# Performance work log

Hardware: AMD Instinct MI355X
Metric: run time of the kernel (lower is better)

The kernel has to match this reference:

```python
import math
import jax, jax.numpy as jnp
import numpy as np

B, T, DIN, D, L, H = 512, 16, 7, 512, 2, 8
FF = 4 * D
HD = D // H
NEG = -1e30


def setup_inputs() -> dict:
    key = jax.random.key(0)
    ks = jax.random.split(key, 18)
    s = 0.02
    n = lambda k, sh: jax.random.normal(k, sh, dtype=jnp.float32) * s
    return {
        "x_scalar_norm": jax.random.normal(ks[0], (B, T, DIN), dtype=jnp.float32),
        "ip_w": n(ks[1], (DIN, D)),   # input_proj (x @ W)
        "ip_b": n(ks[2], (D,)),
        "qkv_w": n(ks[3], (L, D, 3 * D)),  # packed in_proj per layer
        "qkv_b": n(ks[4], (L, 3 * D)),
        "out_w": n(ks[5], (L, D, D)),
        "out_b": n(ks[6], (L, D)),
        "ln1_s": jnp.ones((L, D), jnp.float32),
        "ln1_b": jnp.zeros((L, D), jnp.float32),
        "ff_w1": n(ks[7], (L, D, FF)),
        "ff_b1": n(ks[8], (L, FF)),
        "ff_w2": n(ks[9], (L, FF, D)),
        "ff_b2": n(ks[10], (L, D)),
        "ln2_s": jnp.ones((L, D), jnp.float32),
        "ln2_b": jnp.zeros((L, D), jnp.float32),
        "head_w": n(ks[11], (D, 3)),  # moment_head
        "head_b": n(ks[12], (3,)),
    }


def _pos_encoding(t, d):
    pos = jnp.arange(t, dtype=jnp.float32)[:, None]
    div = jnp.exp(jnp.arange(0, d, 2, dtype=jnp.float32) * (-math.log(10000.0) / d))
    pe = jnp.zeros((t, d), jnp.float32)
    pe = pe.at[:, 0::2].set(jnp.sin(pos * div))
    pe = pe.at[:, 1::2].set(jnp.cos(pos * div))
    return pe


def _ln(x, s, b, eps=1e-5):
    m = jnp.mean(x, axis=-1, keepdims=True)
    v = jnp.mean(jnp.square(x - m), axis=-1, keepdims=True)
    return (x - m) * jax.lax.rsqrt(v + eps) * s + b


def _encoder_layer(h, qkv_w, qkv_b, out_w, out_b, ln1_s, ln1_b,
                   w1, b1, w2, b2, ln2_s, ln2_b, causal):
    b, t, _ = h.shape
    qkv = h @ qkv_w + qkv_b  # [b, t, 3D]
    q, k, v = jnp.split(qkv, 3, axis=-1)
    q = q.reshape(b, t, H, HD).transpose(0, 2, 1, 3)  # bhqd
    k = k.reshape(b, t, H, HD).transpose(0, 2, 1, 3)
    v = v.reshape(b, t, H, HD).transpose(0, 2, 1, 3)
    scores = jnp.einsum('bhqd,bhkd->bhqk', q, k) / math.sqrt(HD)
    scores = jnp.where(causal[None, None], scores, NEG)
    attn = jax.nn.softmax(scores, axis=-1)
    o = jnp.einsum('bhqk,bhkd->bhqd', attn, v)
    o = o.transpose(0, 2, 1, 3).reshape(b, t, D) @ out_w + out_b
    h = _ln(h + o, ln1_s, ln1_b)           # post-norm (norm_first=False)
    ff = jax.nn.relu(h @ w1 + b1) @ w2 + b2
    return _ln(h + ff, ln2_s, ln2_b)


def reference(x_scalar_norm, ip_w, ip_b, qkv_w, qkv_b, out_w, out_b,
              ln1_s, ln1_b, ff_w1, ff_b1, ff_w2, ff_b2, ln2_s, ln2_b,
              head_w, head_b):
    b, t_total, _ = x_scalar_norm.shape
    pe = _pos_encoding(t_total, D)
    x_roll = x_scalar_norm
    preds = []
    for t in range(t_total):
        xp = x_roll[:, :t + 1, :]                 # full backbone recompute per step
        h = xp @ ip_w + ip_b + pe[None, :t + 1]
        causal = jnp.tril(jnp.ones((t + 1, t + 1), dtype=bool))
        for l in range(L):
            h = _encoder_layer(h, qkv_w[l], qkv_b[l], out_w[l], out_b[l],
                               ln1_s[l], ln1_b[l], ff_w1[l], ff_b1[l],
                               ff_w2[l], ff_b2[l], ln2_s[l], ln2_b[l], causal)
        y_t = h[:, -1, :] @ head_w + head_b       # [b, 3]
        preds.append(y_t)
        if t < t_total - 1:
            # eval mode: no teacher forcing; feed back detached prediction
            x_roll = x_roll.at[:, t + 1, DIN - 3:].set(jax.lax.stop_gradient(y_t))
    return jnp.stack(preds, axis=1)  # [b, T, 3]
```

## Files before the change

kernel.cpp:

```cpp
#include <hip/hip_runtime.h>
#include <hip/hip_bf16.h>
#include <math.h>


typedef __attribute__((__ext_vector_type__(8))) short short8;
typedef __attribute__((__ext_vector_type__(4))) float floatx4;

__device__ inline short8 as_short8(uint4 v){ union U{uint4 u; short8 s;} x; x.u=v; return x.s; }

__device__ inline ushort f2bf(float f){
    __hip_bfloat16 h = __float2bfloat16(f);
    ushort u; __builtin_memcpy(&u, &h, 2); return u;
}

__global__ __launch_bounds__(256)
void swz_k(const float* __restrict__ qkv_w, const float* __restrict__ out_w,
           const float* __restrict__ ff1_w, const float* __restrict__ ff2_w,
           ushort* __restrict__ wsw)
{
    int id = blockIdx.z; int l = id & 1; int mi = id >> 1;
    int K, N; const float* src; size_t doff;
    if (mi == 0)      { K = 512;  N = 1536; src = qkv_w + (size_t)l*786432;  doff = (size_t)l*786432; }
    else if (mi == 1) { K = 512;  N = 512;  src = out_w + (size_t)l*262144;  doff = 1572864 + (size_t)l*262144; }
    else if (mi == 2) { K = 512;  N = 2048; src = ff1_w + (size_t)l*1048576; doff = 2097152 + (size_t)l*1048576; }
    else              { K = 2048; N = 512;  src = ff2_w + (size_t)l*1048576; doff = 4194304 + (size_t)l*1048576; }
    int n0 = blockIdx.x * 64, k0 = blockIdx.y * 32;
    if (n0 >= N || k0 >= K) return;
    __shared__ float tt[32][64];
    int tid = threadIdx.x;
    int c = tid & 63, r = tid >> 6;
    #pragma unroll
    for (int i = 0; i < 8; ++i)
        tt[r + i*4][c] = src[(size_t)(k0 + r + i*4)*N + n0 + c];
    __syncthreads();
    int q = tid >> 6, n = tid & 63;
    union { ushort s[8]; uint4 v; } pk;
    #pragma unroll
    for (int i = 0; i < 8; ++i) pk.s[i] = f2bf(tt[q*8 + i][n]);
    ((uint4*)(wsw + doff))[(size_t)((k0 >> 5)*4 + q)*N + n0 + n] = pk.v;
}

__global__ __launch_bounds__(256)
void embed0_k(const float* __restrict__ x, const float* __restrict__ ip_w,
              const float* __restrict__ ip_b, float* __restrict__ h,
              __hip_bfloat16* __restrict__ hbf)
{
    int idx = blockIdx.x*256 + threadIdx.x;
    int b = idx >> 9, d = idx & 511;
    float pe = (d & 1) ? 1.0f : 0.0f;
    float acc = ip_b[d] + pe;
    #pragma unroll
    for (int i = 0; i < 7; ++i)
        acc += x[(b*16 + 0)*7 + i] * ip_w[i*512 + d];
    h[idx] = acc;
    hbf[idx] = __float2bfloat16(acc);
}

template<int MODE>
__global__ __launch_bounds__(256)
void gemm64_k(const __hip_bfloat16* __restrict__ A, const ushort* __restrict__ Wsw,
              const float* __restrict__ bias, int t,
              float* __restrict__ qbuf, __hip_bfloat16* __restrict__ kc,
              __hip_bfloat16* __restrict__ vc,
              __hip_bfloat16* __restrict__ obf, float* __restrict__ ofp,
              const float* __restrict__ resid)
{
    constexpr int K = (MODE == 2) ? 2048 : 512;
    constexpr int N = (MODE == 0) ? 1536 : (MODE == 1 ? 2048 : 512);
    __shared__ uint4 ldsA[256], ldsB[256];
    int tid = threadIdx.x, lane = tid & 63, w = tid >> 6;
    int n0 = blockIdx.x*64, m0 = blockIdx.y*64;
    const uint4* Ag = (const uint4*)A;
    const uint4* Bg = (const uint4*)Wsw;
    int am = tid >> 2, aq = tid & 3;
    int bq = tid >> 6, bn = tid & 63;
    int rh = w & 1, ch = w >> 1;
    int qd = lane >> 4, ln = lane & 15;
    floatx4 a00 = {}, a01 = {}, a10 = {}, a11 = {};
    for (int kb = 0; kb < K/32; ++kb){
        ldsA[aq*64 + am] = Ag[(size_t)(m0 + am)*(K/8) + kb*4 + aq];
        ldsB[bq*64 + bn] = Bg[(size_t)(kb*4 + bq)*N + n0 + bn];
        __syncthreads();
        short8 af0 = as_short8(ldsA[qd*64 + rh*32 +      ln]);
        short8 af1 = as_short8(ldsA[qd*64 + rh*32 + 16 + ln]);
        short8 bf0 = as_short8(ldsB[qd*64 + ch*32 +      ln]);
        short8 bf1 = as_short8(ldsB[qd*64 + ch*32 + 16 + ln]);
        a00 = __builtin_amdgcn_mfma_f32_16x16x32_bf16(af0, bf0, a00, 0, 0, 0);
        a01 = __builtin_amdgcn_mfma_f32_16x16x32_bf16(af0, bf1, a01, 0, 0, 0);
        a10 = __builtin_amdgcn_mfma_f32_16x16x32_bf16(af1, bf0, a10, 0, 0, 0);
        a11 = __builtin_amdgcn_mfma_f32_16x16x32_bf16(af1, bf1, a11, 0, 0, 0);
        __syncthreads();
    }
    floatx4 accs[2][2] = {{a00, a01}, {a10, a11}};
    #pragma unroll
    for (int i = 0; i < 2; ++i){
        #pragma unroll
        for (int j = 0; j < 2; ++j){
            #pragma unroll
            for (int r = 0; r < 4; ++r){
                int m = m0 + rh*32 + i*16 + qd*4 + r;
                int n = n0 + ch*32 + j*16 + ln;
                float v = accs[i][j][r] + bias[n];
                if (MODE == 0){
                    if (n < 512) qbuf[(size_t)m*512 + n] = v;
                    else if (n < 1024){ int z = n - 512;
                        kc[(((size_t)m*8 + (z >> 6))*16 + t)*64 + (z & 63)] = __float2bfloat16(v); }
                    else { int z = n - 1024;
                        vc[(((size_t)m*8 + (z >> 6))*16 + t)*64 + (z & 63)] = __float2bfloat16(v); }
                } else if (MODE == 1){
                    obf[(size_t)m*2048 + n] = __float2bfloat16(fmaxf(v, 0.0f));
                } else {
                    ofp[(size_t)m*512 + n] = v + resid[(size_t)m*512 + n];
                }
            }
        }
    }
}

__global__ __launch_bounds__(256)
void attn_k(const float* __restrict__ qbuf, const __hip_bfloat16* __restrict__ kc,
            const __hip_bfloat16* __restrict__ vc, __hip_bfloat16* __restrict__ attn_o, int t)
{
    int w = blockIdx.x*4 + (threadIdx.x >> 6);
    int lane = threadIdx.x & 63;
    int b = w >> 3, hh = w & 7;
    float qv = qbuf[(size_t)b*512 + hh*64 + lane];
    const __hip_bfloat16* kp = kc + ((size_t)b*8 + hh)*16*64;
    const __hip_bfloat16* vp = vc + ((size_t)b*8 + hh)*16*64;
    float m = -1e30f, s = 0.0f, o = 0.0f;
    for (int j = 0; j <= t; ++j){
        float p = qv * __bfloat162float(kp[j*64 + lane]);
        #pragma unroll
        for (int off = 32; off; off >>= 1) p += __shfl_xor(p, off);
        p *= 0.125f;
        float nm = fmaxf(m, p);
        float sc = expf(m - nm);
        float e  = expf(p - nm);
        s = s*sc + e;
        o = o*sc + e*__bfloat162float(vp[j*64 + lane]);
        m = nm;
    }
    attn_o[(size_t)b*512 + hh*64 + lane] = __float2bfloat16(o / s);
}

__global__ __launch_bounds__(256)
void outln_k(const __hip_bfloat16* __restrict__ Abf, const ushort* __restrict__ Wsw,
             const float* __restrict__ ob, const float* __restrict__ g,
             const float* __restrict__ be, float* __restrict__ h,
             __hip_bfloat16* __restrict__ hbf)
{
    __shared__ uint4 lA[64*17 + 1];
    __shared__ float redS[4][4][4], redQ[4][4][4];
    int tid = threadIdx.x, lane = tid & 63, w = tid >> 6;
    int m0 = blockIdx.x*16;
    const uint4* Ag = (const uint4*)Abf;
    #pragma unroll
    for (int it = 0; it < 4; ++it){
        int m = it*4 + w;
        lA[lane*17 + m] = Ag[(size_t)(m0 + m)*64 + lane];
    }
    __syncthreads();
    const uint4* Bg = (const uint4*)Wsw;
    int qd = lane >> 4, ln = lane & 15;
    floatx4 acc[8] = {};
    for (int kb = 0; kb < 16; ++kb){
        short8 af = as_short8(lA[(kb*4 + qd)*17 + ln]);
        #pragma unroll
        for (int c = 0; c < 8; ++c){
            int n = w*128 + c*16 + ln;
            short8 bf = as_short8(Bg[(size_t)(kb*4 + qd)*512 + n]);
            acc[c] = __builtin_amdgcn_mfma_f32_16x16x32_bf16(af, bf, acc[c], 0, 0, 0);
        }
    }
    float v[8][4];
    float psum[4] = {}, psq[4] = {};
    #pragma unroll
    for (int c = 0; c < 8; ++c){
        #pragma unroll
        for (int r = 0; r < 4; ++r){
            int m = qd*4 + r, n = w*128 + c*16 + ln;
            float xv = acc[c][r] + ob[n] + h[(size_t)(m0 + m)*512 + n];
            v[c][r] = xv; psum[r] += xv; psq[r] += xv*xv;
        }
    }
    #pragma unroll
    for (int off = 1; off < 16; off <<= 1){
        #pragma unroll
        for (int r = 0; r < 4; ++r){ psum[r] += __shfl_xor(psum[r], off); psq[r] += __shfl_xor(psq[r], off); }
    }
    if (ln == 0){
        #pragma unroll
        for (int r = 0; r < 4; ++r){ redS[w][qd][r] = psum[r]; redQ[w][qd][r] = psq[r]; }
    }
    __syncthreads();
    float mean[4], rstd[4];
    #pragma unroll
    for (int r = 0; r < 4; ++r){
        float sm = redS[0][qd][r] + redS[1][qd][r] + redS[2][qd][r] + redS[3][qd][r];
        float sq = redQ[0][qd][r] + redQ[1][qd][r] + redQ[2][qd][r] + redQ[3][qd][r];
        mean[r] = sm * (1.0f/512.0f);
        float var = sq * (1.0f/512.0f) - mean[r]*mean[r];
        rstd[r] = rsqrtf(var + 1e-5f);
    }
    #pragma unroll
    for (int c = 0; c < 8; ++c){
        #pragma unroll
        for (int r = 0; r < 4; ++r){
            int m = qd*4 + r, n = w*128 + c*16 + ln;
            float hn = (v[c][r] - mean[r])*rstd[r]*g[n] + be[n];
            h[(size_t)(m0 + m)*512 + n] = hn;
            hbf[(size_t)(m0 + m)*512 + n] = __float2bfloat16(hn);
        }
    }
}

__global__ __launch_bounds__(256)
void ln2he_k(const float* __restrict__ tmp, const float* __restrict__ g,
             const float* __restrict__ be, float* __restrict__ h,
             __hip_bfloat16* __restrict__ hbf,
             const float* __restrict__ hw, const float* __restrict__ hb,
             const float* __restrict__ x, const float* __restrict__ ip_w,
             const float* __restrict__ ip_b, float* __restrict__ out,
             int t, int dohead)
{
    int b = blockIdx.x, tid = threadIdx.x;
    __shared__ float red[4];
    __shared__ float hred[4][3];
    __shared__ float ybc[3];
    float x0 = tmp[(size_t)b*512 + tid];
    float x1 = tmp[(size_t)b*512 + 256 + tid];
    float s = x0 + x1;
    #pragma unroll
    for (int off = 32; off; off >>= 1) s += __shfl_xor(s, off);
    if ((tid & 63) == 0) red[tid >> 6] = s;
    __syncthreads();
    float mean = (red[0] + red[1] + red[2] + red[3]) * (1.0f/512.0f);
    float d0 = x0 - mean, d1 = x1 - mean;
    float vs = d0*d0 + d1*d1;
    #pragma unroll
    for (int off = 32; off; off >>= 1) vs += __shfl_xor(vs, off);
    __syncthreads();
    if ((tid & 63) == 0) red[tid >> 6] = vs;
    __syncthreads();
    float var = (red[0] + red[1] + red[2] + red[3]) * (1.0f/512.0f);
    float r = rsqrtf(var + 1e-5f);
    float n0_ = d0*r*g[tid]       + be[tid];
    float n1_ = d1*r*g[256 + tid] + be[256 + tid];
    if (!dohead){
        h[(size_t)b*512 + tid] = n0_;
        h[(size_t)b*512 + 256 + tid] = n1_;
        hbf[(size_t)b*512 + tid] = __float2bfloat16(n0_);
        hbf[(size_t)b*512 + 256 + tid] = __float2bfloat16(n1_);
        return;
    }
    float s0 = n0_*hw[tid*3]     + n1_*hw[(tid+256)*3];
    float s1 = n0_*hw[tid*3 + 1] + n1_*hw[(tid+256)*3 + 1];
    float s2 = n0_*hw[tid*3 + 2] + n1_*hw[(tid+256)*3 + 2];
    #pragma unroll
    for (int off = 32; off; off >>= 1){
        s0 += __shfl_xor(s0, off); s1 += __shfl_xor(s1, off); s2 += __shfl_xor(s2, off);
    }
    int w = tid >> 6;
    if ((tid & 63) == 0){ hred[w][0] = s0; hred[w][1] = s1; hred[w][2] = s2; }
    __syncthreads();
    if (tid < 3){
        float y = hred[0][tid] + hred[1][tid] + hred[2][tid] + hred[3][tid] + hb[tid];
        out[((size_t)b*16 + t)*3 + tid] = y;
        ybc[tid] = y;
    }
    __syncthreads();
    if (t < 15){
        float y0 = ybc[0], y1 = ybc[1], y2 = ybc[2];
        #pragma unroll
        for (int half = 0; half < 2; ++half){
            int d = tid + half*256;
            int e = d & ~1;
            float div = expf(-(float)e * (9.210340371976184f / 512.0f));
            float arg = (float)(t + 1) * div;
            float pe = (d & 1) ? cosf(arg) : sinf(arg);
            float acc = ip_b[d] + pe;
            #pragma unroll
            for (int i = 0; i < 4; ++i)
                acc += x[((size_t)b*16 + t + 1)*7 + i] * ip_w[i*512 + d];
            acc += y0*ip_w[4*512 + d] + y1*ip_w[5*512 + d] + y2*ip_w[6*512 + d];
            h[(size_t)b*512 + d] = acc;
            hbf[(size_t)b*512 + d] = __float2bfloat16(acc);
        }
    }
}

extern "C" void kernel_launch(void* const* d_in, const int* in_sizes, int n_in,
                              void* d_out, int out_size, void* d_ws, size_t ws_size,
                              hipStream_t stream)
{
    const float* x     = (const float*)d_in[0];
    const float* ip_w  = (const float*)d_in[1];
    const float* ip_b  = (const float*)d_in[2];
    const float* qkv_w = (const float*)d_in[3];
    const float* qkv_b = (const float*)d_in[4];
    const float* out_w = (const float*)d_in[5];
    const float* out_b = (const float*)d_in[6];
    const float* ln1_s = (const float*)d_in[7];
    const float* ln1_b = (const float*)d_in[8];
    const float* ff_w1 = (const float*)d_in[9];
    const float* ff_b1 = (const float*)d_in[10];
    const float* ff_w2 = (const float*)d_in[11];
    const float* ff_b2 = (const float*)d_in[12];
    const float* ln2_s = (const float*)d_in[13];
    const float* ln2_b = (const float*)d_in[14];
    const float* hw    = (const float*)d_in[15];
    const float* hb    = (const float*)d_in[16];
    float* out = (float*)d_out;

    ushort* wsw = (ushort*)d_ws;
    float* h    = (float*)((char*)d_ws + 12582912);
    float* tmp  = h + 262144;
    float* qbuf = tmp + 262144;
    __hip_bfloat16* hbf    = (__hip_bfloat16*)(qbuf + 262144);
    __hip_bfloat16* attnbf = hbf + 262144;
    __hip_bfloat16* ffbf   = attnbf + 262144;
    __hip_bfloat16* kc     = ffbf + 1048576;
    __hip_bfloat16* vc     = kc + 8388608;
    const int CPL = 4194304;

    swz_k<<<dim3(32, 64, 8), 256, 0, stream>>>(qkv_w, out_w, ff_w1, ff_w2, wsw);
    embed0_k<<<1024, 256, 0, stream>>>(x, ip_w, ip_b, h, hbf);

    for (int t = 0; t < 16; ++t){
        for (int l = 0; l < 2; ++l){
            gemm64_k<0><<<dim3(24, 8), 256, 0, stream>>>(
                hbf, wsw + (size_t)l*786432, qkv_b + l*1536, t,
                qbuf, kc + (size_t)l*CPL, vc + (size_t)l*CPL,
                nullptr, nullptr, nullptr);
            attn_k<<<1024, 256, 0, stream>>>(qbuf, kc + (size_t)l*CPL, vc + (size_t)l*CPL, attnbf, t);
            outln_k<<<32, 256, 0, stream>>>(
                attnbf, wsw + 1572864 + (size_t)l*262144, out_b + l*512,
                ln1_s + l*512, ln1_b + l*512, h, hbf);
            gemm64_k<1><<<dim3(32, 8), 256, 0, stream>>>(
                hbf, wsw + 2097152 + (size_t)l*1048576, ff_b1 + l*2048, t,
                nullptr, nullptr, nullptr, ffbf, nullptr, nullptr);
            gemm64_k<2><<<dim3(8, 8), 256, 0, stream>>>(
                ffbf, wsw + 4194304 + (size_t)l*1048576, ff_b2 + l*512, t,
                nullptr, nullptr, nullptr, nullptr, tmp, h);
            ln2he_k<<<512, 256, 0, stream>>>(
                tmp, ln2_s + l*512, ln2_b + l*512, h, hbf,
                hw, hb, x, ip_w, ip_b, out, t, l == 1);
        }
    }
}
```

Baseline: 2.363 ms.

## Fuse whole autoregressive loop into one persistent per-row-block kernel

Replaces the roughly 192 per-step kernel launches (QKV GEMM, attention, out-proj+LN, FF1, FF2, LN2+head+embed) with a single kernel of 32 blocks × 1024 threads. Each block owns 16 batch rows and runs all timesteps and layers itself, keeping activations in LDS and a per-block global scratch. This removes launch overhead and inter-kernel round trips, since rows are independent across the time loop. The cost is that only 32 workgroups run, so each block streams every weight matrix from L2/HBM per step with low CU occupancy.

```diff
diff --git a/kernel.cpp b/kernel.cpp
--- a/kernel.cpp
+++ b/kernel.cpp
@@ -11,6 +11,9 @@
 __device__ inline ushort f2bf(float f){
     __hip_bfloat16 h = __float2bfloat16(f);
     ushort u; __builtin_memcpy(&u, &h, 2); return u;
+}
+__device__ inline float bf2f(ushort u){
+    __hip_bfloat16 h; __builtin_memcpy(&h, &u, 2); return __bfloat162float(h);
 }
 
 __global__ __launch_bounds__(256)
@@ -40,251 +43,342 @@
     ((uint4*)(wsw + doff))[(size_t)((k0 >> 5)*4 + q)*N + n0 + n] = pk.v;
 }
 
-__global__ __launch_bounds__(256)
-void embed0_k(const float* __restrict__ x, const float* __restrict__ ip_w,
-              const float* __restrict__ ip_b, float* __restrict__ h,
-              __hip_bfloat16* __restrict__ hbf)
+__global__ __launch_bounds__(1024, 1)
+void rowchain_k(const float* __restrict__ x, const ushort* __restrict__ wsw,
+                const float* __restrict__ ip_w, const float* __restrict__ ip_b,
+                const float* __restrict__ qkv_b, const float* __restrict__ out_b,
+                const float* __restrict__ ln1_s, const float* __restrict__ ln1_b,
+                const float* __restrict__ ff_b1, const float* __restrict__ ff_b2,
+                const float* __restrict__ ln2_s, const float* __restrict__ ln2_b,
+                const float* __restrict__ hw, const float* __restrict__ hb,
+                float* __restrict__ out,
+                float* __restrict__ hres_g, ushort* __restrict__ ffb_g,
+                ushort* __restrict__ kc, ushort* __restrict__ vc)
 {
-    int idx = blockIdx.x*256 + threadIdx.x;
-    int b = idx >> 9, d = idx & 511;
-    float pe = (d & 1) ? 1.0f : 0.0f;
-    float acc = ip_b[d] + pe;
-    #pragma unroll
-    for (int i = 0; i < 7; ++i)
-        acc += x[(b*16 + 0)*7 + i] * ip_w[i*512 + d];
-    h[idx] = acc;
-    hbf[idx] = __float2bfloat16(acc);
-}
-
-template<int MODE>
-__global__ __launch_bounds__(256)
-void gemm64_k(const __hip_bfloat16* __restrict__ A, const ushort* __restrict__ Wsw,
-              const float* __restrict__ bias, int t,
-              float* __restrict__ qbuf, __hip_bfloat16* __restrict__ kc,
-              __hip_bfloat16* __restrict__ vc,
-              __hip_bfloat16* __restrict__ obf, float* __restrict__ ofp,
-              const float* __restrict__ resid)
-{
-    constexpr int K = (MODE == 2) ? 2048 : 512;
-    constexpr int N = (MODE == 0) ? 1536 : (MODE == 1 ? 2048 : 512);
-    __shared__ uint4 ldsA[256], ldsB[256];
-    int tid = threadIdx.x, lane = tid & 63, w = tid >> 6;
-    int n0 = blockIdx.x*64, m0 = blockIdx.y*64;
-    const uint4* Ag = (const uint4*)A;
-    const uint4* Bg = (const uint4*)Wsw;
-    int am = tid >> 2, aq = tid & 3;
-    int bq = tid >> 6, bn = tid & 63;
-    int rh = w & 1, ch = w >> 1;
-    int qd = lane >> 4, ln = lane & 15;
-    floatx4 a00 = {}, a01 = {}, a10 = {}, a11 = {};
-    for (int kb = 0; kb < K/32; ++kb){
-        ldsA[aq*64 + am] = Ag[(size_t)(m0 + am)*(K/8) + kb*4 + aq];
-        ldsB[bq*64 + bn] = Bg[(size_t)(kb*4 + bq)*N + n0 + bn];
-        __syncthreads();
-        short8 af0 = as_short8(ldsA[qd*64 + rh*32 +      ln]);
-        short8 af1 = as_short8(ldsA[qd*64 + rh*32 + 16 + ln]);
-        short8 bf0 = as_short8(ldsB[qd*64 + ch*32 +      ln]);
-        short8 bf1 = as_short8(ldsB[qd*64 + ch*32 + 16 + ln]);
-        a00 = __builtin_amdgcn_mfma_f32_16x16x32_bf16(af0, bf0, a00, 0, 0, 0);
-        a01 = __builtin_amdgcn_mfma_f32_16x16x32_bf16(af0, bf1, a01, 0, 0, 0);
-        a10 = __builtin_amdgcn_mfma_f32_16x16x32_bf16(af1, bf0, a10, 0, 0, 0);
-        a11 = __builtin_amdgcn_mfma_f32_16x16x32_bf16(af1, bf1, a11, 0, 0, 0);
-        __syncthreads();
-    }
-    floatx4 accs[2][2] = {{a00, a01}, {a10, a11}};
-    #pragma unroll
-    for (int i = 0; i < 2; ++i){
+    __shared__ uint4 hA[64*17];
+    __shared__ float zq[16*512];
+    __shared__ float pstat[16][16][2];
+    __shared__ float stats[16][2];
+    __shared__ float yacc[16][16][3];
+    __shared__ float ybc[16][3];
+
+    const int tid  = threadIdx.x;
+    const int lane = tid & 63, w = tid >> 6;
+    const int qd   = lane >> 4, li = lane & 15;
+    const int blk  = blockIdx.x;
+    const int pm   = tid & 15, pg = tid >> 4;
+
+    float*  hres = hres_g + blk*8192;
+    ushort* ffb  = ffb_g  + (size_t)blk*32768;
+    const int CPL = 4194304;
+
+    {
+        int b = blk*16 + pm;
         #pragma unroll
-        for (int j = 0; j < 2; ++j){
+        for (int j = 0; j < 8; ++j){
+            int d = pg*8 + j;
+            float pe = (d & 1) ? 1.0f : 0.0f;
+            float acc = ip_b[d] + pe;
             #pragma unroll
-            for (int r = 0; r < 4; ++r){
-                int m = m0 + rh*32 + i*16 + qd*4 + r;
-                int n = n0 + ch*32 + j*16 + ln;
-                float v = accs[i][j][r] + bias[n];
-                if (MODE == 0){
-                    if (n < 512) qbuf[(size_t)m*512 + n] = v;
-                    else if (n < 1024){ int z = n - 512;
-                        kc[(((size_t)m*8 + (z >> 6))*16 + t)*64 + (z & 63)] = __float2bfloat16(v); }
-                    else { int z = n - 1024;
-                        vc[(((size_t)m*8 + (z >> 6))*16 + t)*64 + (z & 63)] = __float2bfloat16(v); }
-                } else if (MODE == 1){
-                    obf[(size_t)m*2048 + n] = __float2bfloat16(fmaxf(v, 0.0f));
-                } else {
-                    ofp[(size_t)m*512 + n] = v + resid[(size_t)m*512 + n];
-                }
-            }
+            for (int i = 0; i < 7; ++i)
+                acc += x[(b*16 + 0)*7 + i] * ip_w[i*512 + d];
+            hres[pm*512 + d] = acc;
         }
     }
-}
-
-__global__ __launch_bounds__(256)
-void attn_k(const float* __restrict__ qbuf, const __hip_bfloat16* __restrict__ kc,
-            const __hip_bfloat16* __restrict__ vc, __hip_bfloat16* __restrict__ attn_o, int t)
-{
-    int w = blockIdx.x*4 + (threadIdx.x >> 6);
-    int lane = threadIdx.x & 63;
-    int b = w >> 3, hh = w & 7;
-    float qv = qbuf[(size_t)b*512 + hh*64 + lane];
-    const __hip_bfloat16* kp = kc + ((size_t)b*8 + hh)*16*64;
-    const __hip_bfloat16* vp = vc + ((size_t)b*8 + hh)*16*64;
-    float m = -1e30f, s = 0.0f, o = 0.0f;
-    for (int j = 0; j <= t; ++j){
-        float p = qv * __bfloat162float(kp[j*64 + lane]);
-        #pragma unroll
-        for (int off = 32; off; off >>= 1) p += __shfl_xor(p, off);
-        p *= 0.125f;
-        float nm = fmaxf(m, p);
-        float sc = expf(m - nm);
-        float e  = expf(p - nm);
-        s = s*sc + e;
-        o = o*sc + e*__bfloat162float(vp[j*64 + lane]);
-        m = nm;
-    }
-    attn_o[(size_t)b*512 + hh*64 + lane] = __float2bfloat16(o / s);
-}
-
-__global__ __launch_bounds__(256)
-void outln_k(const __hip_bfloat16* __restrict__ Abf, const ushort* __restrict__ Wsw,
-             const float* __restrict__ ob, const float* __restrict__ g,
-             const float* __restrict__ be, float* __restrict__ h,
-             __hip_bfloat16* __restrict__ hbf)
-{
-    __shared__ uint4 lA[64*17 + 1];
-    __shared__ float redS[4][4][4], redQ[4][4][4];
-    int tid = threadIdx.x, lane = tid & 63, w = tid >> 6;
-    int m0 = blockIdx.x*16;
-    const uint4* Ag = (const uint4*)Abf;
-    #pragma unroll
-    for (int it = 0; it < 4; ++it){
-        int m = it*4 + w;
-        lA[lane*17 + m] = Ag[(size_t)(m0 + m)*64 + lane];
-    }
     __syncthreads();
-    const uint4* Bg = (const uint4*)Wsw;
-    int qd = lane >> 4, ln = lane & 15;
-    floatx4 acc[8] = {};
-    for (int kb = 0; kb < 16; ++kb){
-        short8 af = as_short8(lA[(kb*4 + qd)*17 + ln]);
-        #pragma unroll
-        for (int c = 0; c < 8; ++c){
-            int n = w*128 + c*16 + ln;
-            short8 bf = as_short8(Bg[(size_t)(kb*4 + qd)*512 + n]);
-            acc[c] = __builtin_amdgcn_mfma_f32_16x16x32_bf16(af, bf, acc[c], 0, 0, 0);
-        }
-    }
-    float v[8][4];
-    float psum[4] = {}, psq[4] = {};
-    #pragma unroll
-    for (int c = 0; c < 8; ++c){
-        #pragma unroll
-        for (int r = 0; r < 4; ++r){
-            int m = qd*4 + r, n = w*128 + c*16 + ln;
-            float xv = acc[c][r] + ob[n] + h[(size_t)(m0 + m)*512 + n];
-            v[c][r] = xv; psum[r] += xv; psq[r] += xv*xv;
-        }
-    }
-    #pragma unroll
-    for (int off = 1; off < 16; off <<= 1){
-        #pragma unroll
-        for (int r = 0; r < 4; ++r){ psum[r] += __shfl_xor(psum[r], off); psq[r] += __shfl_xor(psq[r], off); }
-    }
-    if (ln == 0){
-        #pragma unroll
-        for (int r = 0; r < 4; ++r){ redS[w][qd][r] = psum[r]; redQ[w][qd][r] = psq[r]; }
-    }
-    __syncthreads();
-    float mean[4], rstd[4];
-    #pragma unroll
-    for (int r = 0; r < 4; ++r){
-        float sm = redS[0][qd][r] + redS[1][qd][r] + redS[2][qd][r] + redS[3][qd][r];
-        float sq = redQ[0][qd][r] + redQ[1][qd][r] + redQ[2][qd][r] + redQ[3][qd][r];
-        mean[r] = sm * (1.0f/512.0f);
-        float var = sq * (1.0f/512.0f) - mean[r]*mean[r];
-        rstd[r] = rsqrtf(var + 1e-5f);
-    }
-    #pragma unroll
-    for (int c = 0; c < 8; ++c){
-        #pragma unroll
-        for (int r = 0; r < 4; ++r){
-            int m = qd*4 + r, n = w*128 + c*16 + ln;
-            float hn = (v[c][r] - mean[r])*rstd[r]*g[n] + be[n];
-            h[(size_t)(m0 + m)*512 + n] = hn;
-            hbf[(size_t)(m0 + m)*512 + n] = __float2bfloat16(hn);
-        }
-    }
-}
-
-__global__ __launch_bounds__(256)
-void ln2he_k(const float* __restrict__ tmp, const float* __restrict__ g,
-             const float* __restrict__ be, float* __restrict__ h,
-             __hip_bfloat16* __restrict__ hbf,
-             const float* __restrict__ hw, const float* __restrict__ hb,
-             const float* __restrict__ x, const float* __restrict__ ip_w,
-             const float* __restrict__ ip_b, float* __restrict__ out,
-             int t, int dohead)
-{
-    int b = blockIdx.x, tid = threadIdx.x;
-    __shared__ float red[4];
-    __shared__ float hred[4][3];
-    __shared__ float ybc[3];
-    float x0 = tmp[(size_t)b*512 + tid];
-    float x1 = tmp[(size_t)b*512 + 256 + tid];
-    float s = x0 + x1;
-    #pragma unroll
-    for (int off = 32; off; off >>= 1) s += __shfl_xor(s, off);
-    if ((tid & 63) == 0) red[tid >> 6] = s;
-    __syncthreads();
-    float mean = (red[0] + red[1] + red[2] + red[3]) * (1.0f/512.0f);
-    float d0 = x0 - mean, d1 = x1 - mean;
-    float vs = d0*d0 + d1*d1;
-    #pragma unroll
-    for (int off = 32; off; off >>= 1) vs += __shfl_xor(vs, off);
-    __syncthreads();
-    if ((tid & 63) == 0) red[tid >> 6] = vs;
-    __syncthreads();
-    float var = (red[0] + red[1] + red[2] + red[3]) * (1.0f/512.0f);
-    float r = rsqrtf(var + 1e-5f);
-    float n0_ = d0*r*g[tid]       + be[tid];
-    float n1_ = d1*r*g[256 + tid] + be[256 + tid];
-    if (!dohead){
-        h[(size_t)b*512 + tid] = n0_;
-        h[(size_t)b*512 + 256 + tid] = n1_;
-        hbf[(size_t)b*512 + tid] = __float2bfloat16(n0_);
-        hbf[(size_t)b*512 + 256 + tid] = __float2bfloat16(n1_);
-        return;
-    }
-    float s0 = n0_*hw[tid*3]     + n1_*hw[(tid+256)*3];
-    float s1 = n0_*hw[tid*3 + 1] + n1_*hw[(tid+256)*3 + 1];
-    float s2 = n0_*hw[tid*3 + 2] + n1_*hw[(tid+256)*3 + 2];
-    #pragma unroll
-    for (int off = 32; off; off >>= 1){
-        s0 += __shfl_xor(s0, off); s1 += __shfl_xor(s1, off); s2 += __shfl_xor(s2, off);
-    }
-    int w = tid >> 6;
-    if ((tid & 63) == 0){ hred[w][0] = s0; hred[w][1] = s1; hred[w][2] = s2; }
-    __syncthreads();
-    if (tid < 3){
-        float y = hred[0][tid] + hred[1][tid] + hred[2][tid] + hred[3][tid] + hb[tid];
-        out[((size_t)b*16 + t)*3 + tid] = y;
-        ybc[tid] = y;
-    }
-    __syncthreads();
-    if (t < 15){
-        float y0 = ybc[0], y1 = ybc[1], y2 = ybc[2];
-        #pragma unroll
-        for (int half = 0; half < 2; ++half){
-            int d = tid + half*256;
-            int e = d & ~1;
-            float div = expf(-(float)e * (9.210340371976184f / 512.0f));
-            float arg = (float)(t + 1) * div;
-            float pe = (d & 1) ? cosf(arg) : sinf(arg);
-            float acc = ip_b[d] + pe;
-            #pragma unroll
-            for (int i = 0; i < 4; ++i)
-                acc += x[((size_t)b*16 + t + 1)*7 + i] * ip_w[i*512 + d];
-            acc += y0*ip_w[4*512 + d] + y1*ip_w[5*512 + d] + y2*ip_w[6*512 + d];
-            h[(size_t)b*512 + d] = acc;
-            hbf[(size_t)b*512 + d] = __float2bfloat16(acc);
+
+    for (int t = 0; t < 16; ++t){
+        for (int l = 0; l < 2; ++l){
+            {
+                float4 v0 = *(const float4*)&hres[pm*512 + pg*8];
+                float4 v1 = *(const float4*)&hres[pm*512 + pg*8 + 4];
+                union { ushort s[8]; uint4 u; } pk;
+                pk.s[0]=f2bf(v0.x); pk.s[1]=f2bf(v0.y); pk.s[2]=f2bf(v0.z); pk.s[3]=f2bf(v0.w);
+                pk.s[4]=f2bf(v1.x); pk.s[5]=f2bf(v1.y); pk.s[6]=f2bf(v1.z); pk.s[7]=f2bf(v1.w);
+                hA[pg*17 + pm] = pk.u;
+            }
+            __syncthreads();
+
+            {
+                const uint4* Bg = (const uint4*)(wsw + (size_t)l*786432);
+                const float* qb = qkv_b + l*1536;
+                ushort* kcl = kc + (size_t)l*CPL;
+                ushort* vcl = vc + (size_t)l*CPL;
+                floatx4 acc[6] = {};
+                for (int kb = 0; kb < 16; ++kb){
+                    short8 af = as_short8(hA[(kb*4 + qd)*17 + li]);
+                    #pragma unroll
+                    for (int c = 0; c < 6; ++c){
+                        int n = (w*6 + c)*16 + li;
+                        short8 bf = as_short8(Bg[(size_t)(kb*4 + qd)*1536 + n]);
+                        acc[c] = __builtin_amdgcn_mfma_f32_16x16x32_bf16(af, bf, acc[c], 0, 0, 0);
+                    }
+                }
+                #pragma unroll
+                for (int c = 0; c < 6; ++c){
+                    #pragma unroll
+                    for (int r = 0; r < 4; ++r){
+                        int m = qd*4 + r;
+                        int n = (w*6 + c)*16 + li;
+                        float v = acc[c][r] + qb[n];
+                        if (n < 512){
+                            zq[m*512 + n] = v;
+                        } else if (n < 1024){
+                            int z = n - 512; int b = blk*16 + m;
+                            kcl[(((size_t)b*8 + (z >> 6))*16 + t)*64 + (z & 63)] = f2bf(v);
+                        } else {
+                            int z = n - 1024; int b = blk*16 + m;
+                            vcl[(((size_t)b*8 + (z >> 6))*16 + t)*64 + (z & 63)] = f2bf(v);
+                        }
+                    }
+                }
+            }
+            __syncthreads();
+
+            {
+                const ushort* kcl = kc + (size_t)l*CPL;
+                const ushort* vcl = vc + (size_t)l*CPL;
+                #pragma unroll
+                for (int p = 0; p < 8; ++p){
+                    int pair = w*8 + p;
+                    int bl = pair >> 3, hh = pair & 7;
+                    float qv = zq[bl*512 + hh*64 + lane];
+                    const ushort* kp = kcl + (((size_t)(blk*16 + bl)*8 + hh)*16)*64;
+                    const ushort* vp = vcl + (((size_t)(blk*16 + bl)*8 + hh)*16)*64;
+                    float m_ = -1e30f, s_ = 0.0f, o_ = 0.0f;
+                    for (int j = 0; j <= t; ++j){
+                        float pq = qv * bf2f(kp[j*64 + lane]);
+                        #pragma unroll
+                        for (int off = 32; off; off >>= 1) pq += __shfl_xor(pq, off);
+                        pq *= 0.125f;
+                        float nm = fmaxf(m_, pq);
+                        float sc = expf(m_ - nm);
+                        float e  = expf(pq - nm);
+                        s_ = s_*sc + e;
+                        o_ = o_*sc + e*bf2f(vp[j*64 + lane]);
+                        m_ = nm;
+                    }
+                    int g = hh*8 + (lane >> 3);
+                    ((ushort*)hA)[(g*17 + bl)*8 + (lane & 7)] = f2bf(o_ / s_);
+                }
+            }
+            __syncthreads();
+
+            {
+                const uint4* Bg = (const uint4*)(wsw + 1572864 + (size_t)l*262144);
+                const float* ob = out_b + l*512;
+                floatx4 acc[2] = {};
+                for (int kb = 0; kb < 16; ++kb){
+                    short8 af = as_short8(hA[(kb*4 + qd)*17 + li]);
+                    #pragma unroll
+                    for (int c = 0; c < 2; ++c){
+                        int n = (w*2 + c)*16 + li;
+                        short8 bf = as_short8(Bg[(size_t)(kb*4 + qd)*512 + n]);
+                        acc[c] = __builtin_amdgcn_mfma_f32_16x16x32_bf16(af, bf, acc[c], 0, 0, 0);
+                    }
+                }
+                float ps[4] = {}, pq2[4] = {};
+                #pragma unroll
+                for (int c = 0; c < 2; ++c){
+                    #pragma unroll
+                    for (int r = 0; r < 4; ++r){
+                        int m = qd*4 + r;
+                        int n = (w*2 + c)*16 + li;
+                        float zv = acc[c][r] + ob[n] + hres[m*512 + n];
+                        zq[m*512 + n] = zv;
+                        ps[r] += zv; pq2[r] += zv*zv;
+                    }
+                }
+                #pragma unroll
+                for (int off = 1; off < 16; off <<= 1){
+                    #pragma unroll
+                    for (int r = 0; r < 4; ++r){
+                        ps[r]  += __shfl_xor(ps[r],  off);
+                        pq2[r] += __shfl_xor(pq2[r], off);
+                    }
+                }
+                if (li == 0){
+                    #pragma unroll
+                    for (int r = 0; r < 4; ++r){
+                        pstat[w][qd*4 + r][0] = ps[r];
+                        pstat[w][qd*4 + r][1] = pq2[r];
+                    }
+                }
+            }
+            __syncthreads();
+            if (tid < 16){
+                float s = 0.f, sq = 0.f;
+                #pragma unroll
+                for (int wv = 0; wv < 16; ++wv){ s += pstat[wv][tid][0]; sq += pstat[wv][tid][1]; }
+                float mean = s * (1.0f/512.0f);
+                float var  = sq * (1.0f/512.0f) - mean*mean;
+                stats[tid][0] = mean;
+                stats[tid][1] = rsqrtf(var + 1e-5f);
+            }
+            __syncthreads();
+
+            {
+                const float* g1  = ln1_s + l*512;
+                const float* be1 = ln1_b + l*512;
+                float mean = stats[pm][0], rs = stats[pm][1];
+                float nv[8];
+                #pragma unroll
+                for (int j = 0; j < 8; ++j){
+                    int d = pg*8 + j;
+                    nv[j] = (zq[pm*512 + d] - mean)*rs*g1[d] + be1[d];
+                }
+                *(float4*)&hres[pm*512 + pg*8]     = make_float4(nv[0], nv[1], nv[2], nv[3]);
+                *(float4*)&hres[pm*512 + pg*8 + 4] = make_float4(nv[4], nv[5], nv[6], nv[7]);
+                union { ushort s[8]; uint4 u; } pk;
+                #pragma unroll
+                for (int j = 0; j < 8; ++j) pk.s[j] = f2bf(nv[j]);
+                hA[pg*17 + pm] = pk.u;
+            }
+            __syncthreads();
+
+            {
+                const uint4* Bg = (const uint4*)(wsw + 2097152 + (size_t)l*1048576);
+                const float* fb = ff_b1 + l*2048;
+                floatx4 acc[8] = {};
+                for (int kb = 0; kb < 16; ++kb){
+                    short8 af = as_short8(hA[(kb*4 + qd)*17 + li]);
+                    #pragma unroll
+                    for (int c = 0; c < 8; ++c){
+                        int n = (w*8 + c)*16 + li;
+                        short8 bf = as_short8(Bg[(size_t)(kb*4 + qd)*2048 + n]);
+                        acc[c] = __builtin_amdgcn_mfma_f32_16x16x32_bf16(af, bf, acc[c], 0, 0, 0);
+                    }
+                }
+                #pragma unroll
+                for (int c = 0; c < 8; ++c){
+                    #pragma unroll
+                    for (int r = 0; r < 4; ++r){
+                        int m = qd*4 + r;
+                        int n = (w*8 + c)*16 + li;
+                        float v = acc[c][r] + fb[n];
+                        ffb[m*2048 + n] = f2bf(fmaxf(v, 0.0f));
+                    }
+                }
+            }
+            __syncthreads();
+
+            {
+                const uint4* Bg = (const uint4*)(wsw + 4194304 + (size_t)l*1048576);
+                floatx4 acc[2] = {};
+                for (int chunk = 0; chunk < 4; ++chunk){
+                    if (chunk) __syncthreads();
+                    hA[pg*17 + pm] = *(const uint4*)&ffb[pm*2048 + chunk*512 + pg*8];
+                    __syncthreads();
+                    for (int kb = 0; kb < 16; ++kb){
+                        short8 af = as_short8(hA[(kb*4 + qd)*17 + li]);
+                        #pragma unroll
+                        for (int c = 0; c < 2; ++c){
+                            int n = (w*2 + c)*16 + li;
+                            short8 bf = as_short8(Bg[(size_t)((chunk*16 + kb)*4 + qd)*512 + n]);
+                            acc[c] = __builtin_amdgcn_mfma_f32_16x16x32_bf16(af, bf, acc[c], 0, 0, 0);
+                        }
+                    }
+                }
+                const float* fb = ff_b2 + l*512;
+                float ps[4] = {}, pq2[4] = {};
+                #pragma unroll
+                for (int c = 0; c < 2; ++c){
+                    #pragma unroll
+                    for (int r = 0; r < 4; ++r){
+                        int m = qd*4 + r;
+                        int n = (w*2 + c)*16 + li;
+                        float zv = acc[c][r] + fb[n] + hres[m*512 + n];
+                        zq[m*512 + n] = zv;
+                        ps[r] += zv; pq2[r] += zv*zv;
+                    }
+                }
+                #pragma unroll
+                for (int off = 1; off < 16; off <<= 1){
+                    #pragma unroll
+                    for (int r = 0; r < 4; ++r){
+                        ps[r]  += __shfl_xor(ps[r],  off);
+                        pq2[r] += __shfl_xor(pq2[r], off);
+                    }
+                }
+                if (li == 0){
+                    #pragma unroll
+                    for (int r = 0; r < 4; ++r){
+                        pstat[w][qd*4 + r][0] = ps[r];
+                        pstat[w][qd*4 + r][1] = pq2[r];
+                    }
+                }
+            }
+            __syncthreads();
+            if (tid < 16){
+                float s = 0.f, sq = 0.f;
+                #pragma unroll
+                for (int wv = 0; wv < 16; ++wv){ s += pstat[wv][tid][0]; sq += pstat[wv][tid][1]; }
+                float mean = s * (1.0f/512.0f);
+                float var  = sq * (1.0f/512.0f) - mean*mean;
+                stats[tid][0] = mean;
+                stats[tid][1] = rsqrtf(var + 1e-5f);
+            }
+            __syncthreads();
+
+            {
+                const float* g2  = ln2_s + l*512;
+                const float* be2 = ln2_b + l*512;
+                float mean = stats[pm][0], rs = stats[pm][1];
+                float nv[8];
+                #pragma unroll
+                for (int j = 0; j < 8; ++j){
+                    int d = pg*8 + j;
+                    nv[j] = (zq[pm*512 + d] - mean)*rs*g2[d] + be2[d];
+                }
+                if (l == 0){
+                    *(float4*)&hres[pm*512 + pg*8]     = make_float4(nv[0], nv[1], nv[2], nv[3]);
+                    *(float4*)&hres[pm*512 + pg*8 + 4] = make_float4(nv[4], nv[5], nv[6], nv[7]);
+                } else {
+                    float s0 = 0.f, s1 = 0.f, s2 = 0.f;
+                    #pragma unroll
+                    for (int j = 0; j < 8; ++j){
+                        int d = pg*8 + j;
+                        s0 += nv[j]*hw[d*3 + 0];
+                        s1 += nv[j]*hw[d*3 + 1];
+                        s2 += nv[j]*hw[d*3 + 2];
+                    }
+                    s0 += __shfl_xor(s0, 16); s0 += __shfl_xor(s0, 32);
+                    s1 += __shfl_xor(s1, 16); s1 += __shfl_xor(s1, 32);
+                    s2 += __shfl_xor(s2, 16); s2 += __shfl_xor(s2, 32);
+                    if (lane < 16){
+                        yacc[w][lane][0] = s0; yacc[w][lane][1] = s1; yacc[w][lane][2] = s2;
+                    }
+                    __syncthreads();
+                    if (tid < 48){
+                        int m = tid / 3, k = tid % 3;
+                        float y = hb[k];
+                        #pragma unroll
+                        for (int wv = 0; wv < 16; ++wv) y += yacc[wv][m][k];
+                        out[((size_t)(blk*16 + m)*16 + t)*3 + k] = y;
+                        ybc[m][k] = y;
+                    }
+                    __syncthreads();
+                    if (t < 15){
+                        int b = blk*16 + pm;
+                        float y0 = ybc[pm][0], y1 = ybc[pm][1], y2 = ybc[pm][2];
+                        #pragma unroll
+                        for (int j = 0; j < 8; ++j){
+                            int d = pg*8 + j;
+                            int e = d & ~1;
+                            float div = expf(-(float)e * (9.210340371976184f / 512.0f));
+                            float arg = (float)(t + 1) * div;
+                            float pe = (d & 1) ? cosf(arg) : sinf(arg);
+                            float acc = ip_b[d] + pe;
+                            #pragma unroll
+                            for (int i = 0; i < 4; ++i)
+                                acc += x[((size_t)b*16 + t + 1)*7 + i] * ip_w[i*512 + d];
+                            acc += y0*ip_w[4*512 + d] + y1*ip_w[5*512 + d] + y2*ip_w[6*512 + d];
+                            hres[pm*512 + d] = acc;
+                        }
+                    }
+                }
+            }
+            __syncthreads();
         }
     }
 }
@@ -312,39 +406,16 @@
     const float* hb    = (const float*)d_in[16];
     float* out = (float*)d_out;
 
-    ushort* wsw = (ushort*)d_ws;
-    float* h    = (float*)((char*)d_ws + 12582912);
-    float* tmp  = h + 262144;
-    float* qbuf = tmp + 262144;
-    __hip_bfloat16* hbf    = (__hip_bfloat16*)(qbuf + 262144);
-    __hip_bfloat16* attnbf = hbf + 262144;
-    __hip_bfloat16* ffbf   = attnbf + 262144;
-    __hip_bfloat16* kc     = ffbf + 1048576;
-    __hip_bfloat16* vc     = kc + 8388608;
-    const int CPL = 4194304;
+    ushort* wsw   = (ushort*)d_ws;
+    float* hres_g = (float*)((char*)d_ws + 12582912);
+    ushort* ffb_g = (ushort*)(hres_g + 262144);
+    ushort* kc    = ffb_g + 1048576;
+    ushort* vc    = kc + 8388608;
 
     swz_k<<<dim3(32, 64, 8), 256, 0, stream>>>(qkv_w, out_w, ff_w1, ff_w2, wsw);
-    embed0_k<<<1024, 256, 0, stream>>>(x, ip_w, ip_b, h, hbf);
-
-    for (int t = 0; t < 16; ++t){
-        for (int l = 0; l < 2; ++l){
-            gemm64_k<0><<<dim3(24, 8), 256, 0, stream>>>(
-                hbf, wsw + (size_t)l*786432, qkv_b + l*1536, t,
-                qbuf, kc + (size_t)l*CPL, vc + (size_t)l*CPL,
-                nullptr, nullptr, nullptr);
-            attn_k<<<1024, 256, 0, stream>>>(qbuf, kc + (size_t)l*CPL, vc + (size_t)l*CPL, attnbf, t);
-            outln_k<<<32, 256, 0, stream>>>(
-                attnbf, wsw + 1572864 + (size_t)l*262144, out_b + l*512,
-                ln1_s + l*512, ln1_b + l*512, h, hbf);
-            gemm64_k<1><<<dim3(32, 8), 256, 0, stream>>>(
-                hbf, wsw + 2097152 + (size_t)l*1048576, ff_b1 + l*2048, t,
-                nullptr, nullptr, nullptr, ffbf, nullptr, nullptr);
-            gemm64_k<2><<<dim3(8, 8), 256, 0, stream>>>(
-                ffbf, wsw + 4194304 + (size_t)l*1048576, ff_b2 + l*512, t,
-                nullptr, nullptr, nullptr, nullptr, tmp, h);
-            ln2he_k<<<512, 256, 0, stream>>>(
-                tmp, ln2_s + l*512, ln2_b + l*512, h, hbf,
-                hw, hb, x, ip_w, ip_b, out, t, l == 1);
-        }
-    }
+
+    rowchain_k<<<32, 1024, 0, stream>>>(
+        x, wsw, ip_w, ip_b, qkv_b, out_b, ln1_s, ln1_b,
+        ff_b1, ff_b2, ln2_s, ln2_b, hw, hb, out,
+        hres_g, ffb_g, kc, vc);
 }
```

Measured after the change: 7.397 ms. 3.13x slower.
